# Performance work log

Hardware: AMD Instinct MI355X
Metric: run time of the kernel (lower is better)

The kernel has to match this reference:

```python
import jax, jax.numpy as jnp
import numpy as np

B, S, H, NH = 2, 2048, 1024, 16
D = H // NH
EPS = 1.1920929e-07  # torch fp32 finfo eps used by F.rms_norm default
ROPE_BASE = 10000.0


def setup_inputs() -> dict:
    key = jax.random.key(0)
    k0, k1, k2, k3 = jax.random.split(key, 4)
    return {
        "x": jax.random.normal(k0, (B, S, H), jnp.float32),
        "ve": jax.random.normal(k1, (B, S, H), jnp.float32),
        "W_qkv": jax.random.normal(k2, (3 * H, H), jnp.float32) * 0.02,
        "W_o": jax.random.normal(k3, (H, H), jnp.float32) * 0.02,
        "lambdas": jnp.array([0.5, 0.5], jnp.float32),
    }


def _rms_norm(x):
    # F.rms_norm without learnable weight, over last dim
    return x * jax.lax.rsqrt(jnp.mean(x * x, axis=-1, keepdims=True) + EPS)


def _rope(x):
    # x: [b, s, h, d]; rotate-half style RoPE matching the Rotary module
    d = x.shape[-1]
    inv_freq = (1.0 / ROPE_BASE) ** (jnp.arange(0, d, 2, dtype=jnp.float32) / d)
    t = jnp.arange(x.shape[1], dtype=jnp.float32)
    freqs = t[:, None] * inv_freq[None, :]          # [s, d/2]
    cos = jnp.cos(freqs)[None, :, None, :]
    sin = jnp.sin(freqs)[None, :, None, :]
    x1, x2 = jnp.split(x, 2, axis=-1)
    return jnp.concatenate([x1 * cos + x2 * sin, -x1 * sin + x2 * cos], axis=-1)


def reference(x, ve, W_qkv, W_o, lambdas):
    qkv = x @ W_qkv.T                                # [b, s, 3H]
    q, k, v = jnp.split(qkv, 3, axis=-1)
    rs = lambda a: a.reshape(B, S, NH, D)            # b s (h d) -> b s h d
    q, k, v = rs(q), rs(k), rs(v)
    q = _rope(_rms_norm(q))
    k = _rope(_rms_norm(k))
    v = lambdas[0] * v + lambdas[1] * rs(ve)         # value-lambda mix
    scale = 1.0 / jnp.sqrt(jnp.asarray(D, jnp.float32))  # flex_attention default
    scores = jnp.einsum('bqhd,bkhd->bhqk', q, k) * scale
    causal = jnp.tril(jnp.ones((S, S), bool))
    scores = jnp.where(causal[None, None], scores, jnp.asarray(-jnp.inf, scores.dtype))
    p = jax.nn.softmax(scores, axis=-1)
    a = jnp.einsum('bhqk,bkhd->bqhd', p, v).reshape(B, S, H)
    return a @ W_o.T
```

## Files before the change

### kernel.cpp

```cpp
#include <hip/hip_runtime.h>
#include <math.h>

typedef __bf16 bf16;
typedef __attribute__((ext_vector_type(8))) __bf16 bf16x8;
typedef __attribute__((ext_vector_type(4))) __bf16 bf16x4;
typedef __attribute__((ext_vector_type(4))) float f32x4;

#define B_  2
#define S_  2048
#define H_  1024
#define NH_ 16
#define D_  64

__device__ __forceinline__ f32x4 mfma16(bf16x8 a, bf16x8 b, f32x4 c) {
    return __builtin_amdgcn_mfma_f32_16x16x32_bf16(a, b, c, 0, 0, 0);
}

__device__ __forceinline__ void async16(void* lds, const void* g) {
    __builtin_amdgcn_global_load_lds(
        (const __attribute__((address_space(1))) unsigned int*)g,
        (__attribute__((address_space(3))) unsigned int*)lds, 16, 0, 0);
}

__global__ __launch_bounds__(256) void cvt_main(
    const float* __restrict__ x, const float* __restrict__ wqkv,
    bf16* __restrict__ xb, bf16* __restrict__ wqb, float2* __restrict__ tab)
{
    const int bid = blockIdx.x, tid = threadIdx.x;
    if (bid < 4096) {
        int i = bid * 256 + tid;
        f32x4 v = *(const f32x4*)(x + (size_t)i * 4);
        bf16x4 o; o[0]=(bf16)v[0]; o[1]=(bf16)v[1]; o[2]=(bf16)v[2]; o[3]=(bf16)v[3];
        *(bf16x4*)(xb + (size_t)i * 4) = o;
    } else if (bid < 7168) {
        int i = (bid - 4096) * 256 + tid;
        f32x4 v = *(const f32x4*)(wqkv + (size_t)i * 4);
        bf16x4 o; o[0]=(bf16)v[0]; o[1]=(bf16)v[1]; o[2]=(bf16)v[2]; o[3]=(bf16)v[3];
        *(bf16x4*)(wqb + (size_t)i * 4) = o;
    } else {
        int idx = (bid - 7168) * 256 + tid;
        int s = idx >> 5, i = idx & 31;
        float f = exp2f((float)i * (-13.287712379549449f / 32.0f));
        float sn, cs;
        sincosf((float)s * f, &sn, &cs);
        tab[idx] = make_float2(cs, sn);
    }
}

__global__ __launch_bounds__(256) void cvt_bf16(const float* __restrict__ src,
                                                bf16* __restrict__ dst, int n4) {
    int i = blockIdx.x * 256 + threadIdx.x;
    if (i >= n4) return;
    f32x4 v = *(const f32x4*)(src + (size_t)i * 4);
    bf16x4 o; o[0]=(bf16)v[0]; o[1]=(bf16)v[1]; o[2]=(bf16)v[2]; o[3]=(bf16)v[3];
    *(bf16x4*)(dst + (size_t)i * 4) = o;
}

__global__ __launch_bounds__(512, 2) void gemm_qkv(
    const bf16* __restrict__ A, const bf16* __restrict__ W,
    bf16* __restrict__ qb, bf16* __restrict__ kb, bf16* __restrict__ vtb,
    const float* __restrict__ ve, const float* __restrict__ lambdas,
    const float2* __restrict__ tab)
{
    constexpr int K  = H_;
    constexpr int NS = K >> 6;
    __shared__ bf16 Al[2][256][64];
    __shared__ bf16 Bl[2][256][64];
    const int id = blockIdx.x + 12 * blockIdx.y;
    const int rX = id & 7, qX = id >> 3;
    const int m0 = ((rX >> 2) * 8 + qX / 3) * 256;
    const int n0 = ((rX & 3) * 3 + qX % 3) * 256;
    const int tid  = threadIdx.x;
    const int lane = tid & 63;
    const int w    = tid >> 6;
    const int quad = lane >> 4;
    const int l16  = lane & 15;
    const int l7r  = l16 & 7;
    const int wm   = (w >> 2) * 128;
    const int wn   = (w & 3) * 64;
    const int r8   = lane >> 3;
    const int cs   = ((lane & 7) ^ r8) * 8;

    auto stage_half = [&](int sl, int kt, int h) {
        const int k0 = kt << 6;
        if (h < 2) {
            const bf16* g = A + (size_t)(m0 + h * 128 + w * 16 + r8) * K + k0 + cs;
            async16(&Al[sl][h * 128 + w * 16][0],     g);
            async16(&Al[sl][h * 128 + w * 16 + 8][0], g + (size_t)8 * K);
        } else {
            const bf16* g = W + (size_t)(n0 + (h - 2) * 128 + w * 16 + r8) * K + k0 + cs;
            async16(&Bl[sl][(h - 2) * 128 + w * 16][0],     g);
            async16(&Bl[sl][(h - 2) * 128 + w * 16 + 8][0], g + (size_t)8 * K);
        }
    };

    const f32x4 Z4 = {0.f, 0.f, 0.f, 0.f};
    f32x4 acc[8][4];
#pragma unroll
    for (int i = 0; i < 8; ++i)
#pragma unroll
        for (int j = 0; j < 4; ++j) acc[i][j] = Z4;

    stage_half(0, 0, 0); stage_half(0, 0, 1); stage_half(0, 0, 2); stage_half(0, 0, 3);
    stage_half(1, (NS > 1 ? 1 : 0), 0);

    for (int t = 0; t < NS; ++t) {
        const int cur = t & 1;
        const int kt1 = (t + 1 < NS) ? t + 1 : NS - 1;
        const int kt2 = (t + 2 < NS) ? t + 2 : NS - 1;
        bf16x8 aL[4][2], aH[4][2], bq0[2][2], bq1[2][2];

        asm volatile("s_waitcnt vmcnt(2)" ::: "memory");
        __builtin_amdgcn_s_barrier();
#pragma unroll
        for (int ks = 0; ks < 2; ++ks) {
#pragma unroll
            for (int i = 0; i < 4; ++i)
                aL[i][ks] = *(const bf16x8*)
                    &Al[cur][wm + i * 16 + l16][(((ks << 2) + quad) ^ l7r) * 8];
#pragma unroll
            for (int j = 0; j < 2; ++j)
                bq0[j][ks] = *(const bf16x8*)
                    &Bl[cur][wn + j * 16 + l16][(((ks << 2) + quad) ^ l7r) * 8];
        }
        stage_half(cur ^ 1, kt1, 1);
        __builtin_amdgcn_s_setprio(1);
#pragma unroll
        for (int ks = 0; ks < 2; ++ks)
#pragma unroll
            for (int i = 0; i < 4; ++i)
#pragma unroll
                for (int j = 0; j < 2; ++j)
                    acc[i][j] = mfma16(aL[i][ks], bq0[j][ks], acc[i][j]);
        __builtin_amdgcn_s_setprio(0);

        __builtin_amdgcn_s_barrier();
#pragma unroll
        for (int ks = 0; ks < 2; ++ks)
#pragma unroll
            for (int j = 0; j < 2; ++j)
                bq1[j][ks] = *(const bf16x8*)
                    &Bl[cur][wn + 32 + j * 16 + l16][(((ks << 2) + quad) ^ l7r) * 8];
        stage_half(cur ^ 1, kt1, 2);
        __builtin_amdgcn_s_setprio(1);
#pragma unroll
        for (int ks = 0; ks < 2; ++ks)
#pragma unroll
            for (int i = 0; i < 4; ++i)
#pragma unroll
                for (int j = 0; j < 2; ++j)
                    acc[i][2 + j] = mfma16(aL[i][ks], bq1[j][ks], acc[i][2 + j]);
        __builtin_amdgcn_s_setprio(0);

        __builtin_amdgcn_s_barrier();
#pragma unroll
        for (int ks = 0; ks < 2; ++ks)
#pragma unroll
            for (int i = 0; i < 4; ++i)
                aH[i][ks] = *(const bf16x8*)
                    &Al[cur][wm + 64 + i * 16 + l16][(((ks << 2) + quad) ^ l7r) * 8];
        stage_half(cur ^ 1, kt1, 3);
        __builtin_amdgcn_s_setprio(1);
#pragma unroll
        for (int ks = 0; ks < 2; ++ks)
#pragma unroll
            for (int i = 0; i < 4; ++i)
#pragma unroll
                for (int j = 0; j < 2; ++j)
                    acc[4 + i][j] = mfma16(aH[i][ks], bq0[j][ks], acc[4 + i][j]);
        __builtin_amdgcn_s_setprio(0);

        __builtin_amdgcn_s_barrier();
        stage_half(cur, kt2, 0);
        __builtin_amdgcn_s_setprio(1);
#pragma unroll
        for (int ks = 0; ks < 2; ++ks)
#pragma unroll
            for (int i = 0; i < 4; ++i)
#pragma unroll
                for (int j = 0; j < 2; ++j)
                    acc[4 + i][2 + j] = mfma16(aH[i][ks], bq1[j][ks], acc[4 + i][2 + j]);
        __builtin_amdgcn_s_setprio(0);
    }
    asm volatile("s_waitcnt vmcnt(0)" ::: "memory");

    const int nbase = n0 + wn;
    const int which = nbase >> 10;
    const int h     = (nbase & (H_ - 1)) >> 6;
    if (which < 2) {
        bf16* dst = which ? kb : qb;
#pragma unroll
        for (int i = 0; i < 8; ++i) {
            float ss[4];
#pragma unroll
            for (int r = 0; r < 4; ++r)
                ss[r] = acc[i][0][r] * acc[i][0][r] + acc[i][1][r] * acc[i][1][r]
                      + acc[i][2][r] * acc[i][2][r] + acc[i][3][r] * acc[i][3][r];
#pragma unroll
            for (int r = 0; r < 4; ++r) {
                ss[r] += __shfl_xor(ss[r], 1);
                ss[r] += __shfl_xor(ss[r], 2);
                ss[r] += __shfl_xor(ss[r], 4);
                ss[r] += __shfl_xor(ss[r], 8);
            }
#pragma unroll
            for (int r = 0; r < 4; ++r) {
                int    m   = m0 + wm + i * 16 + quad * 4 + r;
                int    bb  = m >> 11, s = m & (S_ - 1);
                float  rms = rsqrtf(ss[r] * (1.0f / 64.0f) + 1.1920929e-07f);
                float  x0 = acc[i][0][r] * rms, x1 = acc[i][1][r] * rms;
                float  x2 = acc[i][2][r] * rms, x3 = acc[i][3][r] * rms;
                float2 t0 = tab[(size_t)s * 32 + l16];
                float2 t1 = tab[(size_t)s * 32 + 16 + l16];
                bf16*  bp = dst + ((size_t)(bb * NH_ + h) * S_ + s) * D_;
                bp[l16]      = (bf16)(x0 * t0.x + x2 * t0.y);
                bp[16 + l16] = (bf16)(x1 * t1.x + x3 * t1.y);
                bp[32 + l16] = (bf16)(x2 * t0.x - x0 * t0.y);
                bp[48 + l16] = (bf16)(x3 * t1.x - x1 * t1.y);
            }
        }
    } else {
        const float l0 = lambdas[0], l1 = lambdas[1];
#pragma unroll
        for (int i = 0; i < 8; ++i) {
            const int m00 = m0 + wm + i * 16 + quad * 4;
            const int bb  = m00 >> 11, s = m00 & (S_ - 1);
#pragma unroll
            for (int j = 0; j < 4; ++j) {
                const int d = j * 16 + l16;
                bf16x4 pk;
#pragma unroll
                for (int r = 0; r < 4; ++r) {
                    float vm = l0 * acc[i][j][r]
                             + l1 * ve[(size_t)(m00 + r) * H_ + h * 64 + d];
                    pk[r] = (bf16)vm;
                }
                *(bf16x4*)&vtb[((size_t)(bb * NH_ + h) * D_ + d) * S_ + s] = pk;
            }
        }
    }
}

template <int EPI, int NT>
__global__ __launch_bounds__(256) void gemm_bt(
    const bf16* __restrict__ A, const bf16* __restrict__ W,
    int M, int N, int K,
    float* __restrict__ outF)
{
    constexpr int JN = NT / 32;
    __shared__ bf16 Al[128][64];
    __shared__ bf16 Bl[NT][64];
    const int id = blockIdx.x + 16 * blockIdx.y;
    const int rX = id & 7, qX = id >> 3;
    const int m0 = ((rX >> 2) * 16 + (qX >> 2)) * 128;
    const int n0 = ((rX & 3) * 4 + (qX & 3)) * NT;
    const int tid  = threadIdx.x;
    const int lane = tid & 63;
    const int w    = tid >> 6;
    const int quad = lane >> 4;
    const int l16  = lane & 15;
    const int wm   = (w >> 1) * 64;
    const int wn   = (w & 1) * (NT / 2);
    const int r8   = lane >> 3;
    const int cs   = ((lane & 7) ^ r8) * 8;

    const f32x4 Z4 = {0.f, 0.f, 0.f, 0.f};
    f32x4 acc[4][JN];
#pragma unroll
    for (int i = 0; i < 4; ++i)
#pragma unroll
        for (int j = 0; j < JN; ++j) acc[i][j] = Z4;

    for (int k0 = 0; k0 < K; k0 += 64) {
        {
            const bf16* gA = A + (size_t)(m0 + w * 32 + r8) * K + k0 + cs;
            async16(&Al[w * 32][0],      gA);
            async16(&Al[w * 32 + 8][0],  gA + (size_t)8  * K);
            async16(&Al[w * 32 + 16][0], gA + (size_t)16 * K);
            async16(&Al[w * 32 + 24][0], gA + (size_t)24 * K);
        }
        {
            const bf16* gB = W + (size_t)(n0 + w * 16 + r8) * K + k0 + cs;
            async16(&Bl[w * 16][0],     gB);
            async16(&Bl[w * 16 + 8][0], gB + (size_t)8 * K);
        }
        __syncthreads();
#pragma unroll
        for (int ks = 0; ks < 2; ++ks) {
            bf16x8 af[4], bfg[JN];
#pragma unroll
            for (int i = 0; i < 4; ++i)
                af[i] = *(const bf16x8*)
                    &Al[wm + i * 16 + l16][(((ks << 2) + quad) ^ (l16 & 7)) * 8];
#pragma unroll
            for (int j = 0; j < JN; ++j)
                bfg[j] = *(const bf16x8*)
                    &Bl[wn + j * 16 + l16][(((ks << 2) + quad) ^ (l16 & 7)) * 8];
#pragma unroll
            for (int i = 0; i < 4; ++i)
#pragma unroll
                for (int j = 0; j < JN; ++j)
                    acc[i][j] = mfma16(af[i], bfg[j], acc[i][j]);
        }
        __syncthreads();
    }

#pragma unroll
    for (int i = 0; i < 4; ++i)
#pragma unroll
        for (int j = 0; j < JN; ++j)
#pragma unroll
            for (int r = 0; r < 4; ++r) {
                int m = m0 + wm + i * 16 + quad * 4 + r;
                int n = n0 + wn + j * 16 + l16;
                outF[(size_t)m * N + n] = acc[i][j][r];
            }
}

__global__ __launch_bounds__(256) void attn(
    const bf16* __restrict__ Q, const bf16* __restrict__ Kg,
    const bf16* __restrict__ Vt, bf16* __restrict__ Og)
{
    __shared__ bf16 Kl[2][64][64];
    __shared__ bf16 Vl[2][64][64];
    __shared__ bf16 Pl[4][16][64];

    const int bh   = blockIdx.x;
    const int b    = bh >> 4;
    const int h    = bh & 15;
    const int tid  = threadIdx.x;
    const int lane = tid & 63;
    const int w    = tid >> 6;
    const int quad = lane >> 4;
    const int l16  = lane & 15;
    const int l7   = l16 & 7;

    const bf16* Qp = Q  + (size_t)bh * S_ * D_;
    const bf16* Kp = Kg + (size_t)bh * S_ * D_;
    const bf16* Vp = Vt + (size_t)bh * D_ * S_;

    const int srow = lane >> 3;
    const int schk = (lane & 7) ^ (lane >> 3);
    const f32x4 Z4 = {0.f, 0.f, 0.f, 0.f};
    const float C1 = 0.18033688011112042f;
    const float C2 = -11.541560327111707f;

    auto stage = [&](int p, int kb0) {
        const bf16* gK = Kp + (size_t)(kb0 + w * 16 + srow) * D_ + schk * 8;
        async16(&Kl[p][w * 16][0], gK);
        async16(&Kl[p][w * 16 + 8][0], gK + (size_t)8 * D_);
        const bf16* gV = Vp + (size_t)(w * 16 + srow) * S_ + kb0 + schk * 8;
        async16(&Vl[p][w * 16][0], gV);
        async16(&Vl[p][w * 16 + 8][0], gV + (size_t)8 * S_);
    };

    for (int half = 0; half < 2; ++half) {
        const int qt    = half ? (31 - blockIdx.y) : blockIdx.y;
        const int qbase = qt * 64 + w * 16;
        const int qi    = qbase + l16;

        bf16x8 qf0 = *(const bf16x8*)(Qp + (size_t)(qbase + l16) * D_ + quad * 8);
        bf16x8 qf1 = *(const bf16x8*)(Qp + (size_t)(qbase + l16) * D_ + 32 + quad * 8);

        f32x4 of[4];
#pragma unroll
        for (int dt = 0; dt < 4; ++dt) of[dt] = Z4;
        float lsum = 0.f;

        const int nch = qt + 1;
        __syncthreads();
        stage(0, 0);
        for (int c = 0; c < nch; ++c) {
            const int p   = c & 1;
            const int kb0 = c * 64;
            __syncthreads();
            if (c + 1 < nch) stage(p ^ 1, kb0 + 64);

            float ps = 0.f;
            if (c < qt) {
#pragma unroll
                for (int nt = 0; nt < 4; ++nt) {
                    bf16x8 kf0 = *(const bf16x8*)&Kl[p][nt * 16 + l16][(quad ^ l7) * 8];
                    bf16x8 kf1 = *(const bf16x8*)&Kl[p][nt * 16 + l16][((quad + 4) ^ l7) * 8];
                    f32x4 sacc = Z4;
                    sacc = mfma16(kf0, qf0, sacc);
                    sacc = mfma16(kf1, qf1, sacc);
                    bf16x4 pk;
#pragma unroll
                    for (int r = 0; r < 4; ++r) {
                        float pv = exp2f(fmaf(sacc[r], C1, C2));
                        ps += pv;
                        pk[r] = (bf16)pv;
                    }
                    *(bf16x4*)&Pl[w][l16][((nt * 2 + (quad >> 1)) ^ l7) * 8 + (quad & 1) * 4] = pk;
                }
            } else {
#pragma unroll
                for (int nt = 0; nt < 4; ++nt) {
                    bf16x8 kf0 = *(const bf16x8*)&Kl[p][nt * 16 + l16][(quad ^ l7) * 8];
                    bf16x8 kf1 = *(const bf16x8*)&Kl[p][nt * 16 + l16][((quad + 4) ^ l7) * 8];
                    f32x4 sacc = Z4;
                    sacc = mfma16(kf0, qf0, sacc);
                    sacc = mfma16(kf1, qf1, sacc);
                    bf16x4 pk;
#pragma unroll
                    for (int r = 0; r < 4; ++r) {
                        int   key = kb0 + nt * 16 + quad * 4 + r;
                        float pv  = (key <= qi) ? exp2f(fmaf(sacc[r], C1, C2)) : 0.f;
                        ps += pv;
                        pk[r] = (bf16)pv;
                    }
                    *(bf16x4*)&Pl[w][l16][((nt * 2 + (quad >> 1)) ^ l7) * 8 + (quad & 1) * 4] = pk;
                }
            }
            ps += __shfl_xor(ps, 16);
            ps += __shfl_xor(ps, 32);
            lsum += ps;

            bf16x8 pf0 = *(const bf16x8*)&Pl[w][l16][(quad ^ l7) * 8];
            bf16x8 pf1 = *(const bf16x8*)&Pl[w][l16][((quad + 4) ^ l7) * 8];
#pragma unroll
            for (int dt = 0; dt < 4; ++dt) {
                bf16x8 vf0 = *(const bf16x8*)&Vl[p][dt * 16 + l16][(quad ^ l7) * 8];
                bf16x8 vf1 = *(const bf16x8*)&Vl[p][dt * 16 + l16][((quad + 4) ^ l7) * 8];
                of[dt] = mfma16(pf0, vf0, of[dt]);
                of[dt] = mfma16(pf1, vf1, of[dt]);
            }
        }

#pragma unroll
        for (int r = 0; r < 4; ++r) {
            float ld = __shfl(lsum, quad * 4 + r);
            float rl = 1.0f / ld;
            int   qq = qbase + quad * 4 + r;
#pragma unroll
            for (int dt = 0; dt < 4; ++dt)
                Og[((size_t)(b * S_ + qq)) * H_ + h * D_ + dt * 16 + l16] =
                    (bf16)(of[dt][r] * rl);
        }
    }
}

extern "C" void kernel_launch(void* const* d_in, const int* in_sizes, int n_in,
                              void* d_out, int out_size, void* d_ws, size_t ws_size,
                              hipStream_t stream)
{
    const float* x       = (const float*)d_in[0];
    const float* ve      = (const float*)d_in[1];
    const float* Wqkv    = (const float*)d_in[2];
    const float* Wo      = (const float*)d_in[3];
    const float* lambdas = (const float*)d_in[4];
    float* out = (float*)d_out;

    char* od = (char*)d_out;
    char* ws = (char*)d_ws;
    const size_t MB = 1024 * 1024;
    bf16*   xb  = (bf16*)(od);
    bf16*   wqb = (bf16*)(od + 8 * MB);
    float2* tab = (float2*)(od + 14 * MB);
    bf16*   qb  = (bf16*)(ws);
    bf16*   kb  = (bf16*)(ws + 8 * MB);
    bf16*   vtb = (bf16*)(ws + 16 * MB);
    bf16*   ao  = (bf16*)(ws + 24 * MB);
    bf16*   wob = (bf16*)(ws);

    cvt_main<<<7424, 256, 0, stream>>>(x, Wqkv, xb, wqb, tab);
    gemm_qkv<<<dim3(12, 16), 512, 0, stream>>>(
        xb, wqb, qb, kb, vtb, ve, lambdas, (const float2*)tab);
    attn<<<dim3(32, 16), 256, 0, stream>>>(qb, kb, vtb, ao);
    cvt_bf16<<<1024, 256, 0, stream>>>(Wo, wob, (H_ * H_) / 4);
    gemm_bt<1, 64><<<dim3(16, 32), 256, 0, stream>>>(
        ao, wob, B_ * S_, H_, H_, out);
}
```

Measured before the change: 202.0 us.

## Restructure QKV GEMM main loop into unrolled ping-pong double-buffer schedule

Rewrites the QKV projection GEMM's K loop to process two K-tiles per iteration, with fixed LDS buffer indices and a reordered schedule of async global-to-LDS stages. It prefetches both buffers up front and adds extra barriers plus lgkmcnt waits around each MFMA phase. The aim is deeper overlap of global loads with MFMA work and less index arithmetic. The cost is more barriers per tile, which may add synchronisation stalls, and a vmcnt accounting that must be exactly right.

```diff
diff --git a/kernel.cpp b/kernel.cpp
--- a/kernel.cpp
+++ b/kernel.cpp
@@ -56,14 +56,18 @@
     *(bf16x4*)(dst + (size_t)i * 4) = o;
 }
 
+#define PH_BAR __builtin_amdgcn_s_barrier()
+#define LGKM0  asm volatile("s_waitcnt lgkmcnt(0)" ::: "memory")
+
 __global__ __launch_bounds__(512, 2) void gemm_qkv(
     const bf16* __restrict__ A, const bf16* __restrict__ W,
     bf16* __restrict__ qb, bf16* __restrict__ kb, bf16* __restrict__ vtb,
     const float* __restrict__ ve, const float* __restrict__ lambdas,
     const float2* __restrict__ tab)
 {
-    constexpr int K  = H_;
-    constexpr int NS = K >> 6;
+    constexpr int K   = H_;
+    constexpr int NS  = K >> 6;
+    constexpr int NIT = NS >> 1;
     __shared__ bf16 Al[2][256][64];
     __shared__ bf16 Bl[2][256][64];
     const int id = blockIdx.x + 12 * blockIdx.y;
@@ -102,28 +106,28 @@
         for (int j = 0; j < 4; ++j) acc[i][j] = Z4;
 
     stage_half(0, 0, 0); stage_half(0, 0, 1); stage_half(0, 0, 2); stage_half(0, 0, 3);
-    stage_half(1, (NS > 1 ? 1 : 0), 0);
-
-    for (int t = 0; t < NS; ++t) {
-        const int cur = t & 1;
-        const int kt1 = (t + 1 < NS) ? t + 1 : NS - 1;
-        const int kt2 = (t + 2 < NS) ? t + 2 : NS - 1;
+    stage_half(1, 1, 0); stage_half(1, 1, 1); stage_half(1, 1, 2); stage_half(1, 1, 3);
+    asm volatile("s_waitcnt vmcnt(8)" ::: "memory");
+    __builtin_amdgcn_s_barrier();
+
+    for (int it = 0; it < NIT; ++it) {
+        const int t1k  = 2 * it + 1;
+        const bool last = (it == NIT - 1);
         bf16x8 aL[4][2], aH[4][2], bq0[2][2], bq1[2][2];
 
-        asm volatile("s_waitcnt vmcnt(2)" ::: "memory");
-        __builtin_amdgcn_s_barrier();
 #pragma unroll
         for (int ks = 0; ks < 2; ++ks) {
 #pragma unroll
             for (int i = 0; i < 4; ++i)
                 aL[i][ks] = *(const bf16x8*)
-                    &Al[cur][wm + i * 16 + l16][(((ks << 2) + quad) ^ l7r) * 8];
+                    &Al[0][wm + i * 16 + l16][(((ks << 2) + quad) ^ l7r) * 8];
 #pragma unroll
             for (int j = 0; j < 2; ++j)
                 bq0[j][ks] = *(const bf16x8*)
-                    &Bl[cur][wn + j * 16 + l16][(((ks << 2) + quad) ^ l7r) * 8];
-        }
-        stage_half(cur ^ 1, kt1, 1);
+                    &Bl[0][wn + j * 16 + l16][(((ks << 2) + quad) ^ l7r) * 8];
+        }
+        if (it > 0) stage_half(1, t1k, 0);
+        PH_BAR; LGKM0;
         __builtin_amdgcn_s_setprio(1);
 #pragma unroll
         for (int ks = 0; ks < 2; ++ks)
@@ -133,15 +137,16 @@
                 for (int j = 0; j < 2; ++j)
                     acc[i][j] = mfma16(aL[i][ks], bq0[j][ks], acc[i][j]);
         __builtin_amdgcn_s_setprio(0);
-
-        __builtin_amdgcn_s_barrier();
+        PH_BAR;
+
 #pragma unroll
         for (int ks = 0; ks < 2; ++ks)
 #pragma unroll
             for (int j = 0; j < 2; ++j)
                 bq1[j][ks] = *(const bf16x8*)
-                    &Bl[cur][wn + 32 + j * 16 + l16][(((ks << 2) + quad) ^ l7r) * 8];
-        stage_half(cur ^ 1, kt1, 2);
+                    &Bl[0][wn + 32 + j * 16 + l16][(((ks << 2) + quad) ^ l7r) * 8];
+        if (it > 0) stage_half(1, t1k, 1);
+        PH_BAR; LGKM0;
         __builtin_amdgcn_s_setprio(1);
 #pragma unroll
         for (int ks = 0; ks < 2; ++ks)
@@ -151,15 +156,16 @@
                 for (int j = 0; j < 2; ++j)
                     acc[i][2 + j] = mfma16(aL[i][ks], bq1[j][ks], acc[i][2 + j]);
         __builtin_amdgcn_s_setprio(0);
-
-        __builtin_amdgcn_s_barrier();
+        PH_BAR;
+
 #pragma unroll
         for (int ks = 0; ks < 2; ++ks)
 #pragma unroll
             for (int i = 0; i < 4; ++i)
                 aH[i][ks] = *(const bf16x8*)
-                    &Al[cur][wm + 64 + i * 16 + l16][(((ks << 2) + quad) ^ l7r) * 8];
-        stage_half(cur ^ 1, kt1, 3);
+                    &Al[0][wm + 64 + i * 16 + l16][(((ks << 2) + quad) ^ l7r) * 8];
+        if (2 * it + 2 < NS) stage_half(0, 2 * it + 2, 2);
+        PH_BAR; LGKM0;
         __builtin_amdgcn_s_setprio(1);
 #pragma unroll
         for (int ks = 0; ks < 2; ++ks)
@@ -169,9 +175,10 @@
                 for (int j = 0; j < 2; ++j)
                     acc[4 + i][j] = mfma16(aH[i][ks], bq0[j][ks], acc[4 + i][j]);
         __builtin_amdgcn_s_setprio(0);
-
-        __builtin_amdgcn_s_barrier();
-        stage_half(cur, kt2, 0);
+        PH_BAR;
+
+        if (2 * it + 2 < NS) stage_half(0, 2 * it + 2, 3);
+        PH_BAR; LGKM0;
         __builtin_amdgcn_s_setprio(1);
 #pragma unroll
         for (int ks = 0; ks < 2; ++ks)
@@ -181,8 +188,87 @@
                 for (int j = 0; j < 2; ++j)
                     acc[4 + i][2 + j] = mfma16(aH[i][ks], bq1[j][ks], acc[4 + i][2 + j]);
         __builtin_amdgcn_s_setprio(0);
+        if (last) { asm volatile("s_waitcnt vmcnt(0)" ::: "memory"); }
+        else      { asm volatile("s_waitcnt vmcnt(4)" ::: "memory"); }
+        PH_BAR;
+
+#pragma unroll
+        for (int ks = 0; ks < 2; ++ks) {
+#pragma unroll
+            for (int i = 0; i < 4; ++i)
+                aL[i][ks] = *(const bf16x8*)
+                    &Al[1][wm + i * 16 + l16][(((ks << 2) + quad) ^ l7r) * 8];
+#pragma unroll
+            for (int j = 0; j < 2; ++j)
+                bq0[j][ks] = *(const bf16x8*)
+                    &Bl[1][wn + j * 16 + l16][(((ks << 2) + quad) ^ l7r) * 8];
+        }
+        if (2 * it + 2 < NS) stage_half(0, 2 * it + 2, 0);
+        PH_BAR; LGKM0;
+        __builtin_amdgcn_s_setprio(1);
+#pragma unroll
+        for (int ks = 0; ks < 2; ++ks)
+#pragma unroll
+            for (int i = 0; i < 4; ++i)
+#pragma unroll
+                for (int j = 0; j < 2; ++j)
+                    acc[i][j] = mfma16(aL[i][ks], bq0[j][ks], acc[i][j]);
+        __builtin_amdgcn_s_setprio(0);
+        PH_BAR;
+
+#pragma unroll
+        for (int ks = 0; ks < 2; ++ks)
+#pragma unroll
+            for (int j = 0; j < 2; ++j)
+                bq1[j][ks] = *(const bf16x8*)
+                    &Bl[1][wn + 32 + j * 16 + l16][(((ks << 2) + quad) ^ l7r) * 8];
+        if (2 * it + 2 < NS) stage_half(0, 2 * it + 2, 1);
+        PH_BAR; LGKM0;
+        __builtin_amdgcn_s_setprio(1);
+#pragma unroll
+        for (int ks = 0; ks < 2; ++ks)
+#pragma unroll
+            for (int i = 0; i < 4; ++i)
+#pragma unroll
+                for (int j = 0; j < 2; ++j)
+                    acc[i][2 + j] = mfma16(aL[i][ks], bq1[j][ks], acc[i][2 + j]);
+        __builtin_amdgcn_s_setprio(0);
+        PH_BAR;
+
+#pragma unroll
+        for (int ks = 0; ks < 2; ++ks)
+#pragma unroll
+            for (int i = 0; i < 4; ++i)
+                aH[i][ks] = *(const bf16x8*)
+                    &Al[1][wm + 64 + i * 16 + l16][(((ks << 2) + quad) ^ l7r) * 8];
+        if (2 * it + 3 < NS) stage_half(1, 2 * it + 3, 2);
+        PH_BAR; LGKM0;
+        __builtin_amdgcn_s_setprio(1);
+#pragma unroll
+        for (int ks = 0; ks < 2; ++ks)
+#pragma unroll
+            for (int i = 0; i < 4; ++i)
+#pragma unroll
+                for (int j = 0; j < 2; ++j)
+                    acc[4 + i][j] = mfma16(aH[i][ks], bq0[j][ks], acc[4 + i][j]);
+        __builtin_amdgcn_s_setprio(0);
+        PH_BAR;
+
+        if (2 * it + 3 < NS) stage_half(1, 2 * it + 3, 3);
+        PH_BAR; LGKM0;
+        __builtin_amdgcn_s_setprio(1);
+#pragma unroll
+        for (int ks = 0; ks < 2; ++ks)
+#pragma unroll
+            for (int i = 0; i < 4; ++i)
+#pragma unroll
+                for (int j = 0; j < 2; ++j)
+                    acc[4 + i][2 + j] = mfma16(aH[i][ks], bq1[j][ks], acc[4 + i][2 + j]);
+        __builtin_amdgcn_s_setprio(0);
+        if (last) { asm volatile("s_waitcnt vmcnt(0)" ::: "memory"); }
+        else      { asm volatile("s_waitcnt vmcnt(4)" ::: "memory"); }
+        PH_BAR;
     }
-    asm volatile("s_waitcnt vmcnt(0)" ::: "memory");
 
     const int nbase = n0 + wn;
     const int which = nbase >> 10;
```

Result: slower. 213.6 us (+5.7%).

## Load K/V fragments directly from global memory and launch one block per query tile

Applied to the files above, without the earlier changes.

The attention kernel stops staging K and V tiles into double-buffered shared memory with async loads and barriers. Each wave now reads its K and V MFMA fragments straight from global memory, relying on L2/L1 caching across the four waves. The two-tiles-per-block causal load-balancing pairing is removed in favour of a grid of 32x32 blocks with one query tile each. This removes LDS traffic and block-wide syncs, but each wave now loads K/V redundantly from cache with no software prefetch, and the causal imbalance across blocks returns.

```diff
diff --git a/kernel.cpp b/kernel.cpp
--- a/kernel.cpp
+++ b/kernel.cpp
@@ -321,13 +321,12 @@
     const bf16* __restrict__ Q, const bf16* __restrict__ Kg,
     const bf16* __restrict__ Vt, bf16* __restrict__ Og)
 {
-    __shared__ bf16 Kl[2][64][64];
-    __shared__ bf16 Vl[2][64][64];
     __shared__ bf16 Pl[4][16][64];
 
     const int bh   = blockIdx.x;
     const int b    = bh >> 4;
     const int h    = bh & 15;
+    const int qt   = blockIdx.y;
     const int tid  = threadIdx.x;
     const int lane = tid & 63;
     const int w    = tid >> 6;
@@ -339,105 +338,94 @@
     const bf16* Kp = Kg + (size_t)bh * S_ * D_;
     const bf16* Vp = Vt + (size_t)bh * D_ * S_;
 
-    const int srow = lane >> 3;
-    const int schk = (lane & 7) ^ (lane >> 3);
     const f32x4 Z4 = {0.f, 0.f, 0.f, 0.f};
     const float C1 = 0.18033688011112042f;
     const float C2 = -11.541560327111707f;
 
-    auto stage = [&](int p, int kb0) {
-        const bf16* gK = Kp + (size_t)(kb0 + w * 16 + srow) * D_ + schk * 8;
-        async16(&Kl[p][w * 16][0], gK);
-        async16(&Kl[p][w * 16 + 8][0], gK + (size_t)8 * D_);
-        const bf16* gV = Vp + (size_t)(w * 16 + srow) * S_ + kb0 + schk * 8;
-        async16(&Vl[p][w * 16][0], gV);
-        async16(&Vl[p][w * 16 + 8][0], gV + (size_t)8 * S_);
-    };
-
-    for (int half = 0; half < 2; ++half) {
-        const int qt    = half ? (31 - blockIdx.y) : blockIdx.y;
-        const int qbase = qt * 64 + w * 16;
-        const int qi    = qbase + l16;
-
-        bf16x8 qf0 = *(const bf16x8*)(Qp + (size_t)(qbase + l16) * D_ + quad * 8);
-        bf16x8 qf1 = *(const bf16x8*)(Qp + (size_t)(qbase + l16) * D_ + 32 + quad * 8);
-
-        f32x4 of[4];
-#pragma unroll
-        for (int dt = 0; dt < 4; ++dt) of[dt] = Z4;
-        float lsum = 0.f;
-
-        const int nch = qt + 1;
-        __syncthreads();
-        stage(0, 0);
-        for (int c = 0; c < nch; ++c) {
-            const int p   = c & 1;
-            const int kb0 = c * 64;
-            __syncthreads();
-            if (c + 1 < nch) stage(p ^ 1, kb0 + 64);
-
-            float ps = 0.f;
-            if (c < qt) {
-#pragma unroll
-                for (int nt = 0; nt < 4; ++nt) {
-                    bf16x8 kf0 = *(const bf16x8*)&Kl[p][nt * 16 + l16][(quad ^ l7) * 8];
-                    bf16x8 kf1 = *(const bf16x8*)&Kl[p][nt * 16 + l16][((quad + 4) ^ l7) * 8];
-                    f32x4 sacc = Z4;
-                    sacc = mfma16(kf0, qf0, sacc);
-                    sacc = mfma16(kf1, qf1, sacc);
-                    bf16x4 pk;
-#pragma unroll
-                    for (int r = 0; r < 4; ++r) {
-                        float pv = exp2f(fmaf(sacc[r], C1, C2));
-                        ps += pv;
-                        pk[r] = (bf16)pv;
-                    }
-                    *(bf16x4*)&Pl[w][l16][((nt * 2 + (quad >> 1)) ^ l7) * 8 + (quad & 1) * 4] = pk;
+    const int qbase = qt * 64 + w * 16;
+    const int qi    = qbase + l16;
+
+    const bf16x8 qf0 = *(const bf16x8*)(Qp + (size_t)(qbase + l16) * D_ + quad * 8);
+    const bf16x8 qf1 = *(const bf16x8*)(Qp + (size_t)(qbase + l16) * D_ + 32 + quad * 8);
+
+    f32x4 of[4];
+#pragma unroll
+    for (int dt = 0; dt < 4; ++dt) of[dt] = Z4;
+    float lsum = 0.f;
+
+    const int nch = qt + 1;
+    for (int c = 0; c < nch; ++c) {
+        const int kb0 = c * 64;
+
+        bf16x8 vf0[4], vf1[4];
+#pragma unroll
+        for (int dt = 0; dt < 4; ++dt) {
+            const bf16* vp = Vp + (size_t)(dt * 16 + l16) * S_ + kb0;
+            vf0[dt] = *(const bf16x8*)(vp + quad * 8);
+            vf1[dt] = *(const bf16x8*)(vp + 32 + quad * 8);
+        }
+
+        float ps = 0.f;
+        if (c < qt) {
+#pragma unroll
+            for (int nt = 0; nt < 4; ++nt) {
+                const bf16* kp = Kp + (size_t)(kb0 + nt * 16 + l16) * D_;
+                bf16x8 kf0 = *(const bf16x8*)(kp + quad * 8);
+                bf16x8 kf1 = *(const bf16x8*)(kp + 32 + quad * 8);
+                f32x4 sacc = Z4;
+                sacc = mfma16(kf0, qf0, sacc);
+                sacc = mfma16(kf1, qf1, sacc);
+                bf16x4 pk;
+#pragma unroll
+                for (int r = 0; r < 4; ++r) {
+                    float pv = exp2f(fmaf(sacc[r], C1, C2));
+                    ps += pv;
+                    pk[r] = (bf16)pv;
                 }
-            } else {
-#pragma unroll
-                for (int nt = 0; nt < 4; ++nt) {
-                    bf16x8 kf0 = *(const bf16x8*)&Kl[p][nt * 16 + l16][(quad ^ l7) * 8];
-                    bf16x8 kf1 = *(const bf16x8*)&Kl[p][nt * 16 + l16][((quad + 4) ^ l7) * 8];
-                    f32x4 sacc = Z4;
-                    sacc = mfma16(kf0, qf0, sacc);
-                    sacc = mfma16(kf1, qf1, sacc);
-                    bf16x4 pk;
-#pragma unroll
-                    for (int r = 0; r < 4; ++r) {
-                        int   key = kb0 + nt * 16 + quad * 4 + r;
-                        float pv  = (key <= qi) ? exp2f(fmaf(sacc[r], C1, C2)) : 0.f;
-                        ps += pv;
-                        pk[r] = (bf16)pv;
-                    }
-                    *(bf16x4*)&Pl[w][l16][((nt * 2 + (quad >> 1)) ^ l7) * 8 + (quad & 1) * 4] = pk;
+                *(bf16x4*)&Pl[w][l16][((nt * 2 + (quad >> 1)) ^ l7) * 8 + (quad & 1) * 4] = pk;
+            }
+        } else {
+#pragma unroll
+            for (int nt = 0; nt < 4; ++nt) {
+                const bf16* kp = Kp + (size_t)(kb0 + nt * 16 + l16) * D_;
+                bf16x8 kf0 = *(const bf16x8*)(kp + quad * 8);
+                bf16x8 kf1 = *(const bf16x8*)(kp + 32 + quad * 8);
+                f32x4 sacc = Z4;
+                sacc = mfma16(kf0, qf0, sacc);
+                sacc = mfma16(kf1, qf1, sacc);
+                bf16x4 pk;
+#pragma unroll
+                for (int r = 0; r < 4; ++r) {
+                    int   key = kb0 + nt * 16 + quad * 4 + r;
+                    float pv  = (key <= qi) ? exp2f(fmaf(sacc[r], C1, C2)) : 0.f;
+                    ps += pv;
+                    pk[r] = (bf16)pv;
                 }
-            }
-            ps += __shfl_xor(ps, 16);
-            ps += __shfl_xor(ps, 32);
-            lsum += ps;
-
-            bf16x8 pf0 = *(const bf16x8*)&Pl[w][l16][(quad ^ l7) * 8];
-            bf16x8 pf1 = *(const bf16x8*)&Pl[w][l16][((quad + 4) ^ l7) * 8];
-#pragma unroll
-            for (int dt = 0; dt < 4; ++dt) {
-                bf16x8 vf0 = *(const bf16x8*)&Vl[p][dt * 16 + l16][(quad ^ l7) * 8];
-                bf16x8 vf1 = *(const bf16x8*)&Vl[p][dt * 16 + l16][((quad + 4) ^ l7) * 8];
-                of[dt] = mfma16(pf0, vf0, of[dt]);
-                of[dt] = mfma16(pf1, vf1, of[dt]);
-            }
-        }
-
-#pragma unroll
-        for (int r = 0; r < 4; ++r) {
-            float ld = __shfl(lsum, quad * 4 + r);
-            float rl = 1.0f / ld;
-            int   qq = qbase + quad * 4 + r;
-#pragma unroll
-            for (int dt = 0; dt < 4; ++dt)
-                Og[((size_t)(b * S_ + qq)) * H_ + h * D_ + dt * 16 + l16] =
-                    (bf16)(of[dt][r] * rl);
-        }
+                *(bf16x4*)&Pl[w][l16][((nt * 2 + (quad >> 1)) ^ l7) * 8 + (quad & 1) * 4] = pk;
+            }
+        }
+        ps += __shfl_xor(ps, 16);
+        ps += __shfl_xor(ps, 32);
+        lsum += ps;
+
+        bf16x8 pf0 = *(const bf16x8*)&Pl[w][l16][(quad ^ l7) * 8];
+        bf16x8 pf1 = *(const bf16x8*)&Pl[w][l16][((quad + 4) ^ l7) * 8];
+#pragma unroll
+        for (int dt = 0; dt < 4; ++dt) {
+            of[dt] = mfma16(pf0, vf0[dt], of[dt]);
+            of[dt] = mfma16(pf1, vf1[dt], of[dt]);
+        }
+    }
+
+#pragma unroll
+    for (int r = 0; r < 4; ++r) {
+        float ld = __shfl(lsum, quad * 4 + r);
+        float rl = 1.0f / ld;
+        int   qq = qbase + quad * 4 + r;
+#pragma unroll
+        for (int dt = 0; dt < 4; ++dt)
+            Og[((size_t)(b * S_ + qq)) * H_ + h * D_ + dt * 16 + l16] =
+                (bf16)(of[dt][r] * rl);
     }
 }
 
@@ -467,7 +455,7 @@
     cvt_main<<<7424, 256, 0, stream>>>(x, Wqkv, xb, wqb, tab);
     gemm_qkv<<<dim3(12, 16), 512, 0, stream>>>(
         xb, wqb, qb, kb, vtb, ve, lambdas, (const float2*)tab);
-    attn<<<dim3(32, 16), 256, 0, stream>>>(qb, kb, vtb, ao);
+    attn<<<dim3(32, 32), 256, 0, stream>>>(qb, kb, vtb, ao);
     cvt_bf16<<<1024, 256, 0, stream>>>(Wo, wob, (H_ * H_) / 4);
     gemm_bt<1, 64><<<dim3(16, 32), 256, 0, stream>>>(
         ao, wob, B_ * S_, H_, H_, out);
```

Measured after the change: 303.8 us. +50.4%, slower.
